# Performance work log

Measured on AMD Instinct MI355X. Metric: run time of the kernel, lower is better.

The kernel has to match this reference:

```python
import jax, jax.numpy as jnp
import numpy as np

B, N, D, P, H, DH = 1, 1536, 512, 64, 16, 64
INNER = H * DH  # 1024

def _ln(x, g, b, eps=1e-5):
    m = jnp.mean(x, axis=-1, keepdims=True)
    v = jnp.var(x, axis=-1, keepdims=True)
    return (x - m) / jnp.sqrt(v + eps) * g + b

def setup_inputs() -> dict:
    key = jax.random.key(0)
    ks = jax.random.split(key, 10)
    s = 0.02
    return {
        "node_feats": jax.random.normal(ks[0], (B, N, D), jnp.float32),
        "pair_feats": jax.random.normal(ks[1], (B, N, N, P), jnp.float32),
        "mask": jnp.ones((B, N, N), dtype=bool),
        "ln_node_g": jnp.ones((D,), jnp.float32), "ln_node_b": jnp.zeros((D,), jnp.float32),
        "ln_pair_g": jnp.ones((P,), jnp.float32), "ln_pair_b": jnp.zeros((P,), jnp.float32),
        "Wq": s * jax.random.normal(ks[2], (D, INNER), jnp.float32),
        "bq": jnp.zeros((INNER,), jnp.float32),
        "Wkv": s * jax.random.normal(ks[3], (D, 2 * INNER), jnp.float32),
        "bkv": jnp.zeros((2 * INNER,), jnp.float32),
        "qln_g": jnp.ones((INNER,), jnp.float32), "qln_b": jnp.zeros((INNER,), jnp.float32),
        "kln_g": jnp.ones((INNER,), jnp.float32), "kln_b": jnp.zeros((INNER,), jnp.float32),
        "Wg": s * jax.random.normal(ks[4], (D, INNER), jnp.float32),
        "bg": jnp.zeros((INNER,), jnp.float32),
        "Wbias": s * jax.random.normal(ks[5], (P, H), jnp.float32),
        "Wout": s * jax.random.normal(ks[6], (INNER, D), jnp.float32),
        "bout": jnp.zeros((D,), jnp.float32),
        "n_queries": 0,
        "n_keys": 0,
    }

def reference(node_feats, pair_feats, mask, ln_node_g, ln_node_b, ln_pair_g, ln_pair_b,
              Wq, bq, Wkv, bkv, qln_g, qln_b, kln_g, kln_b, Wg, bg, Wbias, Wout, bout,
              n_queries, n_keys):
    b, n, _ = node_feats.shape
    x = _ln(node_feats, ln_node_g, ln_node_b)          # [b,n,D]
    p = _ln(pair_feats, ln_pair_g, ln_pair_b)          # [b,n,n,P]
    q = _ln(x @ Wq + bq, qln_g, qln_b)                 # [b,n,I]
    kv = x @ Wkv + bkv
    k, v = jnp.split(kv, 2, axis=-1)
    k = _ln(k, kln_g, kln_b)
    g = x @ Wg + bg                                    # gating, [b,n,I]
    bias = jnp.einsum('bijp,ph->bhij', p, Wbias)       # pair bias, [b,h,n,n]
    # split heads -> [b,h,n,dh]
    split = lambda t: t.reshape(b, n, H, DH).transpose(0, 2, 1, 3)
    qh, kh, vh, gh = split(q), split(k), split(v), split(g)
    scale = DH ** -0.5
    sim = jnp.einsum('bhid,bhjd->bhij', qh, kh) * scale
    sim = jnp.where(mask[:, None, :, :], sim, jnp.finfo(sim.dtype).min)
    attn = jax.nn.softmax(sim + bias, axis=-1)
    o = jnp.einsum('bhij,bhjd->bhid', attn, vh)        # [b,h,n,dh]
    o = jax.nn.sigmoid(gh) * o
    o = o.transpose(0, 2, 1, 3).reshape(b, n, INNER)
    return o @ Wout + bout
```

## Files before the change

### kernel.cpp

```cpp
#include <hip/hip_runtime.h>

#define NN 1536
#define DD 512
#define PP 64
#define HH 16
#define DHD 64
#define INNER 1024
#define NCHUNK 4
#define JT_PER (NN / 64 / NCHUNK)

typedef __attribute__((ext_vector_type(4))) float f32x4;
typedef __attribute__((ext_vector_type(8))) _Float16 f16x8;
typedef __attribute__((ext_vector_type(4))) _Float16 f16x4;

__device__ inline float wave_sum(float v) {
#pragma unroll
  for (int m = 1; m <= 32; m <<= 1) v += __shfl_xor(v, m);
  return v;
}

__global__ __launch_bounds__(256) void prep_kernel(const float* __restrict__ Wq,
    const float* __restrict__ Wkv, const float* __restrict__ Wg,
    const float* __restrict__ Wout, const float* __restrict__ nf,
    const float* __restrict__ lng, const float* __restrict__ lnb,
    _Float16* __restrict__ BTall, _Float16* __restrict__ WoutT,
    _Float16* __restrict__ x16) {
  int bid = blockIdx.x;
  int tid = threadIdx.x;
  if (bid >= 640) {
    int i = bid - 640;
    int c = tid * 2;
    float2 v = *(const float2*)&nf[(size_t)i * DD + c];
    float s = v.x + v.y, ss = v.x * v.x + v.y * v.y;
    s = wave_sum(s); ss = wave_sum(ss);
    __shared__ float red[2][4];
    int w = tid >> 6;
    if ((tid & 63) == 0) { red[0][w] = s; red[1][w] = ss; }
    __syncthreads();
    s = red[0][0] + red[0][1] + red[0][2] + red[0][3];
    ss = red[1][0] + red[1][1] + red[1][2] + red[1][3];
    float mean = s * (1.f / DD);
    float var = ss * (1.f / DD) - mean * mean;
    float rstd = rsqrtf(var + 1e-5f);
    x16[(size_t)i * DD + c + 0] = (_Float16)((v.x - mean) * rstd * lng[c + 0] + lnb[c + 0]);
    x16[(size_t)i * DD + c + 1] = (_Float16)((v.y - mean) * rstd * lng[c + 1] + lnb[c + 1]);
    return;
  }
  const float* src; int Cs, c0, r0, outStride, outCol; _Float16* dst;
  if (bid < 512) {
    int x = bid & 63, y = bid >> 6;
    int cg0 = x * 64; r0 = y * 64;
    if (cg0 < 1024)      { src = Wq;  Cs = 1024; c0 = cg0; }
    else if (cg0 < 3072) { src = Wkv; Cs = 2048; c0 = cg0 - 1024; }
    else                 { src = Wg;  Cs = 1024; c0 = cg0 - 3072; }
    dst = BTall; outStride = DD; outCol = cg0;
  } else {
    int b = bid - 512;
    int x = b & 7, y = b >> 3;
    c0 = x * 64; r0 = y * 64;
    src = Wout; Cs = DD; dst = WoutT; outStride = INNER; outCol = c0;
  }
  __shared__ float tile[64][65];
  int ri = tid >> 4, ci = (tid & 15) * 4;
#pragma unroll
  for (int p = 0; p < 4; ++p) {
    float4 v = *(const float4*)&src[(size_t)(r0 + ri + p * 16) * Cs + c0 + ci];
    tile[ri + p * 16][ci + 0] = v.x;
    tile[ri + p * 16][ci + 1] = v.y;
    tile[ri + p * 16][ci + 2] = v.z;
    tile[ri + p * 16][ci + 3] = v.w;
  }
  __syncthreads();
  int wr = tid >> 3, wc = (tid & 7) * 8;
#pragma unroll
  for (int p = 0; p < 2; ++p) {
    f16x8 o;
#pragma unroll
    for (int jj = 0; jj < 8; ++jj) o[jj] = (_Float16)tile[wc + jj][wr + p * 32];
    *(f16x8*)&dst[(size_t)(outCol + wr + p * 32) * outStride + r0 + wc] = o;
  }
}

__device__ __forceinline__ void pb_body(int i, int jy, int tid,
    const float* __restrict__ pair, const float* __restrict__ pg,
    const float* __restrict__ pb, const float* __restrict__ Wbias,
    _Float16* __restrict__ bias16) {
  int lane = tid & 63, w = tid >> 6;
  int lj = lane & 15, pbase = (lane >> 4) * 8;
  f16x8 wb0, wb1;
#pragma unroll
  for (int jj = 0; jj < 8; ++jj) {
    wb0[jj] = (_Float16)Wbias[(pbase + jj) * HH + lj];
    wb1[jj] = (_Float16)Wbias[(pbase + 32 + jj) * HH + lj];
  }
  float4 g0 = *(const float4*)&pg[pbase],      g1 = *(const float4*)&pg[pbase + 4];
  float4 g2 = *(const float4*)&pg[pbase + 32], g3 = *(const float4*)&pg[pbase + 36];
  float4 b0 = *(const float4*)&pb[pbase],      b1 = *(const float4*)&pb[pbase + 4];
  float4 b2 = *(const float4*)&pb[pbase + 32], b3 = *(const float4*)&pb[pbase + 36];
  __shared__ _Float16 trans[2][16][72];
  int jbase = jy * 256 + w * 16 + lj;
  const float* src = &pair[((size_t)i * NN + jbase) * PP];
  float4 v0 = *(const float4*)&src[pbase];
  float4 v1 = *(const float4*)&src[pbase + 4];
  float4 v2 = *(const float4*)&src[pbase + 32];
  float4 v3 = *(const float4*)&src[pbase + 36];
  for (int t4 = 0; t4 < 4; ++t4) {
    int jt0 = jy * 256 + t4 * 64;
    float4 n0, n1, n2, n3;
    if (t4 < 3) {
      const float* nsrc = &pair[((size_t)i * NN + jbase + (t4 + 1) * 64) * PP];
      n0 = *(const float4*)&nsrc[pbase];
      n1 = *(const float4*)&nsrc[pbase + 4];
      n2 = *(const float4*)&nsrc[pbase + 32];
      n3 = *(const float4*)&nsrc[pbase + 36];
    }
    float s = v0.x + v0.y + v0.z + v0.w + v1.x + v1.y + v1.z + v1.w
            + v2.x + v2.y + v2.z + v2.w + v3.x + v3.y + v3.z + v3.w;
    float ss = v0.x * v0.x + v0.y * v0.y + v0.z * v0.z + v0.w * v0.w
             + v1.x * v1.x + v1.y * v1.y + v1.z * v1.z + v1.w * v1.w
             + v2.x * v2.x + v2.y * v2.y + v2.z * v2.z + v2.w * v2.w
             + v3.x * v3.x + v3.y * v3.y + v3.z * v3.z + v3.w * v3.w;
    s += __shfl_xor(s, 16); s += __shfl_xor(s, 32);
    ss += __shfl_xor(ss, 16); ss += __shfl_xor(ss, 32);
    float mean = s * (1.f / PP);
    float var = ss * (1.f / PP) - mean * mean;
    float rstd = rsqrtf(var + 1e-5f);
    f16x8 a0, a1;
    a0[0] = (_Float16)((v0.x - mean) * rstd * g0.x + b0.x);
    a0[1] = (_Float16)((v0.y - mean) * rstd * g0.y + b0.y);
    a0[2] = (_Float16)((v0.z - mean) * rstd * g0.z + b0.z);
    a0[3] = (_Float16)((v0.w - mean) * rstd * g0.w + b0.w);
    a0[4] = (_Float16)((v1.x - mean) * rstd * g1.x + b1.x);
    a0[5] = (_Float16)((v1.y - mean) * rstd * g1.y + b1.y);
    a0[6] = (_Float16)((v1.z - mean) * rstd * g1.z + b1.z);
    a0[7] = (_Float16)((v1.w - mean) * rstd * g1.w + b1.w);
    a1[0] = (_Float16)((v2.x - mean) * rstd * g2.x + b2.x);
    a1[1] = (_Float16)((v2.y - mean) * rstd * g2.y + b2.y);
    a1[2] = (_Float16)((v2.z - mean) * rstd * g2.z + b2.z);
    a1[3] = (_Float16)((v2.w - mean) * rstd * g2.w + b2.w);
    a1[4] = (_Float16)((v3.x - mean) * rstd * g3.x + b3.x);
    a1[5] = (_Float16)((v3.y - mean) * rstd * g3.y + b3.y);
    a1[6] = (_Float16)((v3.z - mean) * rstd * g3.z + b3.z);
    a1[7] = (_Float16)((v3.w - mean) * rstd * g3.w + b3.w);
    f32x4 cacc = {};
    cacc = __builtin_amdgcn_mfma_f32_16x16x32_f16(a0, wb0, cacc, 0, 0, 0);
    cacc = __builtin_amdgcn_mfma_f32_16x16x32_f16(a1, wb1, cacc, 0, 0, 0);
#pragma unroll
    for (int rg = 0; rg < 4; ++rg)
      trans[t4 & 1][lj][w * 16 + (lane >> 4) * 4 + rg] = (_Float16)cacc[rg];
    __syncthreads();
    int hh = tid >> 4, jc = (tid & 15) * 4;
    f16x4 ov = *(const f16x4*)&trans[t4 & 1][hh][jc];
    *(f16x4*)&bias16[((size_t)hh * NN + i) * NN + jt0 + jc] = ov;
    v0 = n0; v1 = n1; v2 = n2; v3 = n3;
  }
}

__device__ __forceinline__ void gemm_proj_body(int m0, int n0, int tid,
    const _Float16* __restrict__ A, const _Float16* __restrict__ BT,
    const float* __restrict__ bq, const float* __restrict__ bkv,
    const float* __restrict__ bg, _Float16* __restrict__ C) {
  __shared__ _Float16 As[64][72];
  __shared__ _Float16 Bs[64][72];
  int lane = tid & 63, w = tid >> 6;
  int wm = (w & 1) * 32, wn = (w >> 1) * 32;
  f32x4 acc[2][2] = {};
  int r = tid >> 3, c8 = (tid & 7) * 8;
  int lr = lane & 15, lg = lane >> 4;
  for (int k0 = 0; k0 < DD; k0 += 64) {
    *(f16x8*)&As[r][c8]      = *(const f16x8*)&A[(size_t)(m0 + r) * DD + k0 + c8];
    *(f16x8*)&As[r + 32][c8] = *(const f16x8*)&A[(size_t)(m0 + r + 32) * DD + k0 + c8];
    *(f16x8*)&Bs[r][c8]      = *(const f16x8*)&BT[(size_t)(n0 + r) * DD + k0 + c8];
    *(f16x8*)&Bs[r + 32][c8] = *(const f16x8*)&BT[(size_t)(n0 + r + 32) * DD + k0 + c8];
    __syncthreads();
#pragma unroll
    for (int kf = 0; kf < 2; ++kf) {
      f16x8 a0 = *(const f16x8*)&As[wm + lr][kf * 32 + lg * 8];
      f16x8 a1 = *(const f16x8*)&As[wm + 16 + lr][kf * 32 + lg * 8];
      f16x8 b0 = *(const f16x8*)&Bs[wn + lr][kf * 32 + lg * 8];
      f16x8 b1 = *(const f16x8*)&Bs[wn + 16 + lr][kf * 32 + lg * 8];
      acc[0][0] = __builtin_amdgcn_mfma_f32_16x16x32_f16(a0, b0, acc[0][0], 0, 0, 0);
      acc[0][1] = __builtin_amdgcn_mfma_f32_16x16x32_f16(a0, b1, acc[0][1], 0, 0, 0);
      acc[1][0] = __builtin_amdgcn_mfma_f32_16x16x32_f16(a1, b0, acc[1][0], 0, 0, 0);
      acc[1][1] = __builtin_amdgcn_mfma_f32_16x16x32_f16(a1, b1, acc[1][1], 0, 0, 0);
    }
    __syncthreads();
  }
#pragma unroll
  for (int mi = 0; mi < 2; ++mi)
#pragma unroll
    for (int ni = 0; ni < 2; ++ni)
#pragma unroll
      for (int rg = 0; rg < 4; ++rg) {
        int row = m0 + wm + mi * 16 + lg * 4 + rg;
        int col = n0 + wn + ni * 16 + lr;
        float bv = (col < 1024) ? bq[col] : (col < 3072) ? bkv[col - 1024] : bg[col - 3072];
        C[(size_t)row * 4096 + col] = (_Float16)(acc[mi][ni][rg] + bv);
      }
}

__global__ __launch_bounds__(256) void fat_pb_gemm(const float* __restrict__ pair,
    const float* __restrict__ pg, const float* __restrict__ pb,
    const float* __restrict__ Wbias, _Float16* __restrict__ bias16,
    const _Float16* __restrict__ x16, const _Float16* __restrict__ BTall,
    const float* __restrict__ bq, const float* __restrict__ bkv,
    const float* __restrict__ bg, _Float16* __restrict__ prebuf16) {
  int bid = blockIdx.x;
  int g = bid / 7, r = bid - g * 7;
  int tid = threadIdx.x;
  if (r == 6) {
    gemm_proj_body((g >> 6) * 64, (g & 63) * 64, tid, x16, BTall, bq, bkv, bg, prebuf16);
  } else {
    int p = g * 6 + r;
    int jy = p / NN;
    int i = p - jy * NN;
    pb_body(i, jy, tid, pair, pg, pb, Wbias, bias16);
  }
}

__global__ __launch_bounds__(256) void transpose_f16_b(const _Float16* __restrict__ in0,
    _Float16* __restrict__ out0, int R, int C) {
  const _Float16* in = in0 + (size_t)blockIdx.z * R * C;
  _Float16* out = out0 + (size_t)blockIdx.z * R * C;
  __shared__ _Float16 tile[64][72];
  int c0 = blockIdx.x * 64, r0 = blockIdx.y * 64;
  int tid = threadIdx.x;
  int ri = tid >> 3, ci = (tid & 7) * 8;
#pragma unroll
  for (int p = 0; p < 2; ++p)
    *(f16x8*)&tile[ri + p * 32][ci] = *(const f16x8*)&in[(size_t)(r0 + ri + p * 32) * C + c0 + ci];
  __syncthreads();
#pragma unroll
  for (int p = 0; p < 2; ++p) {
    f16x8 o;
#pragma unroll
    for (int jj = 0; jj < 8; ++jj) o[jj] = tile[ci + jj][ri + p * 32];
    *(f16x8*)&out[(size_t)(c0 + ri + p * 32) * R + r0 + ci] = o;
  }
}

__global__ __launch_bounds__(256) void gemm_f16(const _Float16* __restrict__ A,
    const _Float16* __restrict__ BT, const float* __restrict__ bias,
    float* __restrict__ C, int M, int N, int K) {
  __shared__ _Float16 As[64][72];
  __shared__ _Float16 Bs[64][72];
  int tid = threadIdx.x, lane = tid & 63, w = tid >> 6;
  int m0 = blockIdx.y * 64, n0 = blockIdx.x * 64;
  int wm = (w & 1) * 32, wn = (w >> 1) * 32;
  f32x4 acc[2][2] = {};
  int r = tid >> 3, c8 = (tid & 7) * 8;
  int lr = lane & 15, lg = lane >> 4;
  for (int k0 = 0; k0 < K; k0 += 64) {
    *(f16x8*)&As[r][c8]      = *(const f16x8*)&A[(size_t)(m0 + r) * K + k0 + c8];
    *(f16x8*)&As[r + 32][c8] = *(const f16x8*)&A[(size_t)(m0 + r + 32) * K + k0 + c8];
    *(f16x8*)&Bs[r][c8]      = *(const f16x8*)&BT[(size_t)(n0 + r) * K + k0 + c8];
    *(f16x8*)&Bs[r + 32][c8] = *(const f16x8*)&BT[(size_t)(n0 + r + 32) * K + k0 + c8];
    __syncthreads();
#pragma unroll
    for (int kf = 0; kf < 2; ++kf) {
      f16x8 a0 = *(const f16x8*)&As[wm + lr][kf * 32 + lg * 8];
      f16x8 a1 = *(const f16x8*)&As[wm + 16 + lr][kf * 32 + lg * 8];
      f16x8 b0 = *(const f16x8*)&Bs[wn + lr][kf * 32 + lg * 8];
      f16x8 b1 = *(const f16x8*)&Bs[wn + 16 + lr][kf * 32 + lg * 8];
      acc[0][0] = __builtin_amdgcn_mfma_f32_16x16x32_f16(a0, b0, acc[0][0], 0, 0, 0);
      acc[0][1] = __builtin_amdgcn_mfma_f32_16x16x32_f16(a0, b1, acc[0][1], 0, 0, 0);
      acc[1][0] = __builtin_amdgcn_mfma_f32_16x16x32_f16(a1, b0, acc[1][0], 0, 0, 0);
      acc[1][1] = __builtin_amdgcn_mfma_f32_16x16x32_f16(a1, b1, acc[1][1], 0, 0, 0);
    }
    __syncthreads();
  }
#pragma unroll
  for (int mi = 0; mi < 2; ++mi)
#pragma unroll
    for (int ni = 0; ni < 2; ++ni)
#pragma unroll
      for (int rg = 0; rg < 4; ++rg) {
        int row = m0 + wm + mi * 16 + lg * 4 + rg;
        int col = n0 + wn + ni * 16 + lr;
        C[(size_t)row * N + col] = acc[mi][ni][rg] + bias[col];
      }
}

__global__ __launch_bounds__(256) void qkv_ln_kernel(const _Float16* __restrict__ prebuf,
    const float* __restrict__ qg, const float* __restrict__ qb,
    const float* __restrict__ kg, const float* __restrict__ kb,
    _Float16* __restrict__ q16, _Float16* __restrict__ k16, _Float16* __restrict__ v16) {
  int i = blockIdx.x, tid = threadIdx.x;
  int c = tid * 4;
  const _Float16* rowp = &prebuf[(size_t)i * 4096];
  f16x4 qh = *(const f16x4*)&rowp[c];
  f16x4 kh = *(const f16x4*)&rowp[1024 + c];
  f16x4 vh = *(const f16x4*)&rowp[2048 + c];
  float qv[4], kv[4];
#pragma unroll
  for (int e = 0; e < 4; ++e) { qv[e] = (float)qh[e]; kv[e] = (float)kh[e]; }
  float qs = qv[0] + qv[1] + qv[2] + qv[3];
  float qss = qv[0] * qv[0] + qv[1] * qv[1] + qv[2] * qv[2] + qv[3] * qv[3];
  float ks = kv[0] + kv[1] + kv[2] + kv[3];
  float kss = kv[0] * kv[0] + kv[1] * kv[1] + kv[2] * kv[2] + kv[3] * kv[3];
  qs = wave_sum(qs); qss = wave_sum(qss); ks = wave_sum(ks); kss = wave_sum(kss);
  __shared__ float red[4][4];
  int w = tid >> 6;
  if ((tid & 63) == 0) { red[0][w] = qs; red[1][w] = qss; red[2][w] = ks; red[3][w] = kss; }
  __syncthreads();
  qs = red[0][0] + red[0][1] + red[0][2] + red[0][3];
  qss = red[1][0] + red[1][1] + red[1][2] + red[1][3];
  ks = red[2][0] + red[2][1] + red[2][2] + red[2][3];
  kss = red[3][0] + red[3][1] + red[3][2] + red[3][3];
  float qm = qs * (1.f / INNER), qvr = qss * (1.f / INNER) - qm * qm, qr = rsqrtf(qvr + 1e-5f);
  float km = ks * (1.f / INNER), kvr = kss * (1.f / INNER) - km * km, kr = rsqrtf(kvr + 1e-5f);
  int hh = c >> 6, d = c & 63;
  size_t off = ((size_t)hh * NN + i) * DHD + d;
  f16x4 qo, ko;
#pragma unroll
  for (int e = 0; e < 4; ++e) {
    qo[e] = (_Float16)((qv[e] - qm) * qr * qg[c + e] + qb[c + e]);
    ko[e] = (_Float16)((kv[e] - km) * kr * kg[c + e] + kb[c + e]);
  }
  *(f16x4*)&q16[off] = qo;
  *(f16x4*)&k16[off] = ko;
  *(f16x4*)&v16[off] = vh;
}

__global__ __launch_bounds__(256) void attn_kernel(const _Float16* __restrict__ q16,
    const _Float16* __restrict__ k16, const _Float16* __restrict__ vT16,
    const _Float16* __restrict__ bias16, _Float16* __restrict__ opart,
    float* __restrict__ mlbuf) {
  int it = blockIdx.x, h = blockIdx.y, ck = blockIdx.z;
  int tid = threadIdx.x, lane = tid & 63, w = tid >> 6;
  int lr = lane & 15, lg = lane >> 4;
  __shared__ _Float16 Kt[64][72];
  __shared__ _Float16 Vt[64][72];
  int ib0 = it * 64;
  int ib = ib0 + w * 16;
  f16x8 qb0 = *(const f16x8*)&q16[((size_t)h * NN + ib + lr) * DHD + lg * 8];
  f16x8 qb1 = *(const f16x8*)&q16[((size_t)h * NN + ib + lr) * DHD + 32 + lg * 8];
  float m = -INFINITY, lsum = 0.f;
  f32x4 oacc[4] = {};
  int sr = tid >> 3, sc = (tid & 7) * 8;
  int jt0g = ck * JT_PER;
  const _Float16* brow = &bias16[((size_t)h * NN + ib + lr) * NN];
  f16x8 kA, kB, vA, vB;
  {
    int j0 = jt0g * 64;
    kA = *(const f16x8*)&k16[((size_t)h * NN + j0 + sr) * DHD + sc];
    kB = *(const f16x8*)&k16[((size_t)h * NN + j0 + sr + 32) * DHD + sc];
    vA = *(const f16x8*)&vT16[((size_t)h * DHD + sr) * NN + j0 + sc];
    vB = *(const f16x8*)&vT16[((size_t)h * DHD + sr + 32) * NN + j0 + sc];
  }
  for (int jj = 0; jj < JT_PER; ++jj) {
    int j0 = (jt0g + jj) * 64;
    *(f16x8*)&Kt[sr][sc] = kA;
    *(f16x8*)&Kt[sr + 32][sc] = kB;
    *(f16x8*)&Vt[sr][sc] = vA;
    *(f16x8*)&Vt[sr + 32][sc] = vB;
    f16x4 bl[4];
#pragma unroll
    for (int jq = 0; jq < 4; ++jq)
      bl[jq] = *(const f16x4*)&brow[j0 + jq * 16 + lg * 4];
    __syncthreads();
    if (jj + 1 < JT_PER) {
      int j1 = j0 + 64;
      kA = *(const f16x8*)&k16[((size_t)h * NN + j1 + sr) * DHD + sc];
      kB = *(const f16x8*)&k16[((size_t)h * NN + j1 + sr + 32) * DHD + sc];
      vA = *(const f16x8*)&vT16[((size_t)h * DHD + sr) * NN + j1 + sc];
      vB = *(const f16x8*)&vT16[((size_t)h * DHD + sr + 32) * NN + j1 + sc];
    }
    float s[4][4];
#pragma unroll
    for (int jq = 0; jq < 4; ++jq) {
      f16x8 ka0 = *(const f16x8*)&Kt[jq * 16 + lr][lg * 8];
      f16x8 ka1 = *(const f16x8*)&Kt[jq * 16 + lr][32 + lg * 8];
      f32x4 c = {};
      c = __builtin_amdgcn_mfma_f32_16x16x32_f16(ka0, qb0, c, 0, 0, 0);
      c = __builtin_amdgcn_mfma_f32_16x16x32_f16(ka1, qb1, c, 0, 0, 0);
#pragma unroll
      for (int r = 0; r < 4; ++r)
        s[jq][r] = c[r] * 0.125f + (float)bl[jq][r];
    }
    float tmax = s[0][0];
#pragma unroll
    for (int jq = 0; jq < 4; ++jq)
#pragma unroll
      for (int r = 0; r < 4; ++r) tmax = fmaxf(tmax, s[jq][r]);
    tmax = fmaxf(tmax, __shfl_xor(tmax, 16));
    tmax = fmaxf(tmax, __shfl_xor(tmax, 32));
    float mn = fmaxf(m, tmax);
    float alpha = __expf(m - mn);
    float ps = 0.f;
    f16x4 pf[4];
#pragma unroll
    for (int jq = 0; jq < 4; ++jq)
#pragma unroll
      for (int r = 0; r < 4; ++r) {
        float p = __expf(s[jq][r] - mn);
        ps += p;
        pf[jq][r] = (_Float16)p;
      }
    ps += __shfl_xor(ps, 16);
    ps += __shfl_xor(ps, 32);
    lsum = lsum * alpha + ps;
    m = mn;
    float ar[4];
#pragma unroll
    for (int r = 0; r < 4; ++r) ar[r] = __shfl(alpha, lg * 4 + r);
#pragma unroll
    for (int dt = 0; dt < 4; ++dt)
#pragma unroll
      for (int r = 0; r < 4; ++r) oacc[dt][r] *= ar[r];
#pragma unroll
    for (int dt = 0; dt < 4; ++dt)
#pragma unroll
      for (int jq = 0; jq < 4; ++jq) {
        f16x4 vb = *(const f16x4*)&Vt[dt * 16 + lr][jq * 16 + lg * 4];
        oacc[dt] = __builtin_amdgcn_mfma_f32_16x16x16f16(pf[jq], vb, oacc[dt], 0, 0, 0);
      }
    __syncthreads();
  }
  size_t pbase = (((size_t)it * HH + h) * NCHUNK + ck) * 4096 + (size_t)w * 1024;
#pragma unroll
  for (int dt = 0; dt < 4; ++dt) {
    f16x4 ov;
#pragma unroll
    for (int r = 0; r < 4; ++r) ov[r] = (_Float16)oacc[dt][r];
    *(f16x4*)&opart[pbase + dt * 256 + lane * 4] = ov;
  }
  if (lg == 0) {
    size_t mb = (((size_t)it * HH + h) * NCHUNK + ck) * 128;
    mlbuf[mb + w * 16 + lr] = m;
    mlbuf[mb + 64 + w * 16 + lr] = lsum;
  }
}

__global__ __launch_bounds__(256) void attn_merge(const _Float16* __restrict__ opart,
    const float* __restrict__ mlbuf, const _Float16* __restrict__ prebuf,
    _Float16* __restrict__ o16) {
  int it = blockIdx.x, h = blockIdx.y;
  int tid = threadIdx.x, lane = tid & 63, w = tid >> 6;
  int lr = lane & 15, lg = lane >> 4;
  __shared__ float sm[NCHUNK][64], sl[NCHUNK][64];
  {
    int c = tid >> 6, i = tid & 63;
    size_t mb = (((size_t)it * HH + h) * NCHUNK + c) * 128;
    sm[c][i] = mlbuf[mb + i];
    sl[c][i] = mlbuf[mb + 64 + i];
  }
  __syncthreads();
  float wc[NCHUNK][4], linv[4];
#pragma unroll
  for (int r = 0; r < 4; ++r) {
    int i_loc = w * 16 + lg * 4 + r;
    float mg = sm[0][i_loc];
#pragma unroll
    for (int c = 1; c < NCHUNK; ++c) mg = fmaxf(mg, sm[c][i_loc]);
    float lt = 0.f;
#pragma unroll
    for (int c = 0; c < NCHUNK; ++c) {
      float e = __expf(sm[c][i_loc] - mg);
      wc[c][r] = e;
      lt += e * sl[c][i_loc];
    }
    linv[r] = 1.f / lt;
  }
  size_t base = ((size_t)it * HH + h) * NCHUNK * 4096 + (size_t)w * 1024;
#pragma unroll
  for (int dt = 0; dt < 4; ++dt) {
    float o[4] = {};
#pragma unroll
    for (int c = 0; c < NCHUNK; ++c) {
      f16x4 v = *(const f16x4*)&opart[base + (size_t)c * 4096 + dt * 256 + lane * 4];
#pragma unroll
      for (int r = 0; r < 4; ++r) o[r] += wc[c][r] * (float)v[r];
    }
    int d = dt * 16 + lr;
#pragma unroll
    for (int r = 0; r < 4; ++r) {
      int i = it * 64 + w * 16 + lg * 4 + r;
      float gt = (float)prebuf[(size_t)i * 4096 + 3072 + h * DHD + d];
      float val = o[r] * linv[r] * (1.f / (1.f + __expf(-gt)));
      o16[(size_t)i * INNER + h * DHD + d] = (_Float16)val;
    }
  }
}

extern "C" void kernel_launch(void* const* d_in, const int* in_sizes, int n_in,
                              void* d_out, int out_size, void* d_ws, size_t ws_size,
                              hipStream_t stream) {
  const float* node  = (const float*)d_in[0];
  const float* pair  = (const float*)d_in[1];
  const float* ln_ng = (const float*)d_in[3];
  const float* ln_nb = (const float*)d_in[4];
  const float* ln_pg = (const float*)d_in[5];
  const float* ln_pb = (const float*)d_in[6];
  const float* Wq    = (const float*)d_in[7];
  const float* bq    = (const float*)d_in[8];
  const float* Wkv   = (const float*)d_in[9];
  const float* bkv   = (const float*)d_in[10];
  const float* qlg   = (const float*)d_in[11];
  const float* qlb   = (const float*)d_in[12];
  const float* klg   = (const float*)d_in[13];
  const float* klb   = (const float*)d_in[14];
  const float* Wg    = (const float*)d_in[15];
  const float* bg    = (const float*)d_in[16];
  const float* Wbias = (const float*)d_in[17];
  const float* Wout  = (const float*)d_in[18];
  const float* bout  = (const float*)d_in[19];
  float* out = (float*)d_out;

  char* ws = (char*)d_ws;
  const size_t MB = 1u << 20;
  _Float16* BTall    = (_Float16*)(ws + 0 * MB);
  _Float16* WoutT    = (_Float16*)(ws + 4 * MB);
  _Float16* x16      = (_Float16*)(ws + 5 * MB);
  _Float16* prebuf16 = (_Float16*)(ws + 8 * MB);
  _Float16* q16      = (_Float16*)(ws + 20 * MB);
  _Float16* k16      = (_Float16*)(ws + 23 * MB);
  _Float16* v16      = (_Float16*)(ws + 26 * MB);
  _Float16* vT16     = (_Float16*)(ws + 29 * MB);
  _Float16* o16      = (_Float16*)(ws + 32 * MB);
  _Float16* bias16   = (_Float16*)(ws + 36 * MB);
  _Float16* opart    = (_Float16*)(ws + 112 * MB);
  float*    mlbuf    = (float*)(ws + 126 * MB);

  prep_kernel<<<640 + NN, 256, 0, stream>>>(Wq, Wkv, Wg, Wout, node, ln_ng, ln_nb,
                                            BTall, WoutT, x16);
  fat_pb_gemm<<<10752, 256, 0, stream>>>(pair, ln_pg, ln_pb, Wbias, bias16,
                                         x16, BTall, bq, bkv, bg, prebuf16);
  qkv_ln_kernel<<<NN, 256, 0, stream>>>(prebuf16, qlg, qlb, klg, klb, q16, k16, v16);
  transpose_f16_b<<<dim3(1, NN / 64, HH), 256, 0, stream>>>(v16, vT16, NN, DHD);
  attn_kernel<<<dim3(NN / 64, HH, NCHUNK), 256, 0, stream>>>(q16, k16, vT16, bias16, opart, mlbuf);
  attn_merge<<<dim3(NN / 64, HH), 256, 0, stream>>>(opart, mlbuf, prebuf16, o16);
  gemm_f16<<<dim3(DD / 64, NN / 64), 256, 0, stream>>>(o16, WoutT, bout, out, NN, DD, INNER);
}
```

Baseline: 239.6 us.

## Stagger pair-bias computation across fused kernels to overlap with qkv and attention

Splits the pair-bias LN+projection into four j-quarters of 384 columns each and interleaves them with other work in fused launches. The first two quarters run beside the QKV GEMM, the third beside q/k layernorm and the V transpose (now read straight from prebuf), and the fourth beside the first three attention chunks, whose key ranges only need the already-written bias. The aim is to hide the memory-bound pair read behind compute-bound stages and to drop separate launches and the v16 intermediate. This relies on JT_PER=6 matching the 384-column chunking and on block-index ordering for the data dependencies, with added complexity in the block-to-work mapping.

```diff
diff --git a/kernel.cpp b/kernel.cpp
--- a/kernel.cpp
+++ b/kernel.cpp
@@ -7,7 +7,7 @@
 #define DHD 64
 #define INNER 1024
 #define NCHUNK 4
-#define JT_PER (NN / 64 / NCHUNK)
+#define JT_PER 6
 
 typedef __attribute__((ext_vector_type(4))) float f32x4;
 typedef __attribute__((ext_vector_type(8))) _Float16 f16x8;
@@ -81,7 +81,7 @@
   }
 }
 
-__device__ __forceinline__ void pb_body(int i, int jy, int tid,
+__device__ __forceinline__ void pb_body(int i, int q, int tid,
     const float* __restrict__ pair, const float* __restrict__ pg,
     const float* __restrict__ pb, const float* __restrict__ Wbias,
     _Float16* __restrict__ bias16) {
@@ -98,17 +98,17 @@
   float4 b0 = *(const float4*)&pb[pbase],      b1 = *(const float4*)&pb[pbase + 4];
   float4 b2 = *(const float4*)&pb[pbase + 32], b3 = *(const float4*)&pb[pbase + 36];
   __shared__ _Float16 trans[2][16][72];
-  int jbase = jy * 256 + w * 16 + lj;
+  int jbase = q * 384 + w * 16 + lj;
   const float* src = &pair[((size_t)i * NN + jbase) * PP];
   float4 v0 = *(const float4*)&src[pbase];
   float4 v1 = *(const float4*)&src[pbase + 4];
   float4 v2 = *(const float4*)&src[pbase + 32];
   float4 v3 = *(const float4*)&src[pbase + 36];
-  for (int t4 = 0; t4 < 4; ++t4) {
-    int jt0 = jy * 256 + t4 * 64;
+  for (int t = 0; t < 6; ++t) {
+    int jt0 = q * 384 + t * 64;
     float4 n0, n1, n2, n3;
-    if (t4 < 3) {
-      const float* nsrc = &pair[((size_t)i * NN + jbase + (t4 + 1) * 64) * PP];
+    if (t < 5) {
+      const float* nsrc = &pair[((size_t)i * NN + jbase + (t + 1) * 64) * PP];
       n0 = *(const float4*)&nsrc[pbase];
       n1 = *(const float4*)&nsrc[pbase + 4];
       n2 = *(const float4*)&nsrc[pbase + 32];
@@ -147,10 +147,10 @@
     cacc = __builtin_amdgcn_mfma_f32_16x16x32_f16(a1, wb1, cacc, 0, 0, 0);
 #pragma unroll
     for (int rg = 0; rg < 4; ++rg)
-      trans[t4 & 1][lj][w * 16 + (lane >> 4) * 4 + rg] = (_Float16)cacc[rg];
+      trans[t & 1][lj][w * 16 + (lane >> 4) * 4 + rg] = (_Float16)cacc[rg];
     __syncthreads();
     int hh = tid >> 4, jc = (tid & 15) * 4;
-    f16x4 ov = *(const f16x4*)&trans[t4 & 1][hh][jc];
+    f16x4 ov = *(const f16x4*)&trans[t & 1][hh][jc];
     *(f16x4*)&bias16[((size_t)hh * NN + i) * NN + jt0 + jc] = ov;
     v0 = n0; v1 = n1; v2 = n2; v3 = n3;
   }
@@ -199,98 +199,15 @@
       }
 }
 
-__global__ __launch_bounds__(256) void fat_pb_gemm(const float* __restrict__ pair,
-    const float* __restrict__ pg, const float* __restrict__ pb,
-    const float* __restrict__ Wbias, _Float16* __restrict__ bias16,
-    const _Float16* __restrict__ x16, const _Float16* __restrict__ BTall,
-    const float* __restrict__ bq, const float* __restrict__ bkv,
-    const float* __restrict__ bg, _Float16* __restrict__ prebuf16) {
-  int bid = blockIdx.x;
-  int g = bid / 7, r = bid - g * 7;
-  int tid = threadIdx.x;
-  if (r == 6) {
-    gemm_proj_body((g >> 6) * 64, (g & 63) * 64, tid, x16, BTall, bq, bkv, bg, prebuf16);
-  } else {
-    int p = g * 6 + r;
-    int jy = p / NN;
-    int i = p - jy * NN;
-    pb_body(i, jy, tid, pair, pg, pb, Wbias, bias16);
-  }
-}
-
-__global__ __launch_bounds__(256) void transpose_f16_b(const _Float16* __restrict__ in0,
-    _Float16* __restrict__ out0, int R, int C) {
-  const _Float16* in = in0 + (size_t)blockIdx.z * R * C;
-  _Float16* out = out0 + (size_t)blockIdx.z * R * C;
-  __shared__ _Float16 tile[64][72];
-  int c0 = blockIdx.x * 64, r0 = blockIdx.y * 64;
-  int tid = threadIdx.x;
-  int ri = tid >> 3, ci = (tid & 7) * 8;
-#pragma unroll
-  for (int p = 0; p < 2; ++p)
-    *(f16x8*)&tile[ri + p * 32][ci] = *(const f16x8*)&in[(size_t)(r0 + ri + p * 32) * C + c0 + ci];
-  __syncthreads();
-#pragma unroll
-  for (int p = 0; p < 2; ++p) {
-    f16x8 o;
-#pragma unroll
-    for (int jj = 0; jj < 8; ++jj) o[jj] = tile[ci + jj][ri + p * 32];
-    *(f16x8*)&out[(size_t)(c0 + ri + p * 32) * R + r0 + ci] = o;
-  }
-}
-
-__global__ __launch_bounds__(256) void gemm_f16(const _Float16* __restrict__ A,
-    const _Float16* __restrict__ BT, const float* __restrict__ bias,
-    float* __restrict__ C, int M, int N, int K) {
-  __shared__ _Float16 As[64][72];
-  __shared__ _Float16 Bs[64][72];
-  int tid = threadIdx.x, lane = tid & 63, w = tid >> 6;
-  int m0 = blockIdx.y * 64, n0 = blockIdx.x * 64;
-  int wm = (w & 1) * 32, wn = (w >> 1) * 32;
-  f32x4 acc[2][2] = {};
-  int r = tid >> 3, c8 = (tid & 7) * 8;
-  int lr = lane & 15, lg = lane >> 4;
-  for (int k0 = 0; k0 < K; k0 += 64) {
-    *(f16x8*)&As[r][c8]      = *(const f16x8*)&A[(size_t)(m0 + r) * K + k0 + c8];
-    *(f16x8*)&As[r + 32][c8] = *(const f16x8*)&A[(size_t)(m0 + r + 32) * K + k0 + c8];
-    *(f16x8*)&Bs[r][c8]      = *(const f16x8*)&BT[(size_t)(n0 + r) * K + k0 + c8];
-    *(f16x8*)&Bs[r + 32][c8] = *(const f16x8*)&BT[(size_t)(n0 + r + 32) * K + k0 + c8];
-    __syncthreads();
-#pragma unroll
-    for (int kf = 0; kf < 2; ++kf) {
-      f16x8 a0 = *(const f16x8*)&As[wm + lr][kf * 32 + lg * 8];
-      f16x8 a1 = *(const f16x8*)&As[wm + 16 + lr][kf * 32 + lg * 8];
-      f16x8 b0 = *(const f16x8*)&Bs[wn + lr][kf * 32 + lg * 8];
-      f16x8 b1 = *(const f16x8*)&Bs[wn + 16 + lr][kf * 32 + lg * 8];
-      acc[0][0] = __builtin_amdgcn_mfma_f32_16x16x32_f16(a0, b0, acc[0][0], 0, 0, 0);
-      acc[0][1] = __builtin_amdgcn_mfma_f32_16x16x32_f16(a0, b1, acc[0][1], 0, 0, 0);
-      acc[1][0] = __builtin_amdgcn_mfma_f32_16x16x32_f16(a1, b0, acc[1][0], 0, 0, 0);
-      acc[1][1] = __builtin_amdgcn_mfma_f32_16x16x32_f16(a1, b1, acc[1][1], 0, 0, 0);
-    }
-    __syncthreads();
-  }
-#pragma unroll
-  for (int mi = 0; mi < 2; ++mi)
-#pragma unroll
-    for (int ni = 0; ni < 2; ++ni)
-#pragma unroll
-      for (int rg = 0; rg < 4; ++rg) {
-        int row = m0 + wm + mi * 16 + lg * 4 + rg;
-        int col = n0 + wn + ni * 16 + lr;
-        C[(size_t)row * N + col] = acc[mi][ni][rg] + bias[col];
-      }
-}
-
-__global__ __launch_bounds__(256) void qkv_ln_kernel(const _Float16* __restrict__ prebuf,
+__device__ __forceinline__ void qkv_body(int i, int tid,
+    const _Float16* __restrict__ prebuf,
     const float* __restrict__ qg, const float* __restrict__ qb,
     const float* __restrict__ kg, const float* __restrict__ kb,
-    _Float16* __restrict__ q16, _Float16* __restrict__ k16, _Float16* __restrict__ v16) {
-  int i = blockIdx.x, tid = threadIdx.x;
+    _Float16* __restrict__ q16, _Float16* __restrict__ k16) {
   int c = tid * 4;
   const _Float16* rowp = &prebuf[(size_t)i * 4096];
   f16x4 qh = *(const f16x4*)&rowp[c];
   f16x4 kh = *(const f16x4*)&rowp[1024 + c];
-  f16x4 vh = *(const f16x4*)&rowp[2048 + c];
   float qv[4], kv[4];
 #pragma unroll
   for (int e = 0; e < 4; ++e) { qv[e] = (float)qh[e]; kv[e] = (float)kh[e]; }
@@ -319,15 +236,33 @@
   }
   *(f16x4*)&q16[off] = qo;
   *(f16x4*)&k16[off] = ko;
-  *(f16x4*)&v16[off] = vh;
-}
-
-__global__ __launch_bounds__(256) void attn_kernel(const _Float16* __restrict__ q16,
-    const _Float16* __restrict__ k16, const _Float16* __restrict__ vT16,
-    const _Float16* __restrict__ bias16, _Float16* __restrict__ opart,
-    float* __restrict__ mlbuf) {
-  int it = blockIdx.x, h = blockIdx.y, ck = blockIdx.z;
-  int tid = threadIdx.x, lane = tid & 63, w = tid >> 6;
+}
+
+__device__ __forceinline__ void vt_body(int t, int tid,
+    const _Float16* __restrict__ prebuf, _Float16* __restrict__ vT16) {
+  int z = t / 24, y = t - z * 24;
+  __shared__ _Float16 tile[64][72];
+  int r0 = y * 64;
+  int ri = tid >> 3, ci = (tid & 7) * 8;
+#pragma unroll
+  for (int p = 0; p < 2; ++p)
+    *(f16x8*)&tile[ri + p * 32][ci] =
+        *(const f16x8*)&prebuf[(size_t)(r0 + ri + p * 32) * 4096 + 2048 + z * 64 + ci];
+  __syncthreads();
+#pragma unroll
+  for (int p = 0; p < 2; ++p) {
+    f16x8 o;
+#pragma unroll
+    for (int jj = 0; jj < 8; ++jj) o[jj] = tile[ci + jj][ri + p * 32];
+    *(f16x8*)&vT16[((size_t)z * DHD + ri + p * 32) * NN + r0 + ci] = o;
+  }
+}
+
+__device__ __forceinline__ void attn_body(int it, int h, int ck, int tid,
+    const _Float16* __restrict__ q16, const _Float16* __restrict__ k16,
+    const _Float16* __restrict__ vT16, const _Float16* __restrict__ bias16,
+    _Float16* __restrict__ opart, float* __restrict__ mlbuf) {
+  int lane = tid & 63, w = tid >> 6;
   int lr = lane & 15, lg = lane >> 4;
   __shared__ _Float16 Kt[64][72];
   __shared__ _Float16 Vt[64][72];
@@ -432,6 +367,68 @@
   }
 }
 
+__global__ __launch_bounds__(256) void fat2(const float* __restrict__ pair,
+    const float* __restrict__ pg, const float* __restrict__ pb,
+    const float* __restrict__ Wbias, _Float16* __restrict__ bias16,
+    const _Float16* __restrict__ x16, const _Float16* __restrict__ BTall,
+    const float* __restrict__ bq, const float* __restrict__ bkv,
+    const float* __restrict__ bg, _Float16* __restrict__ prebuf16) {
+  int bid = blockIdx.x;
+  int g = bid / 3, r = bid - g * 3;
+  int tid = threadIdx.x;
+  if (r == 2) {
+    gemm_proj_body((g >> 6) * 64, (g & 63) * 64, tid, x16, BTall, bq, bkv, bg, prebuf16);
+  } else {
+    int p = g * 2 + r;
+    pb_body(p % NN, p / NN, tid, pair, pg, pb, Wbias, bias16);
+  }
+}
+
+__global__ __launch_bounds__(256) void fat3(const float* __restrict__ pair,
+    const float* __restrict__ pg, const float* __restrict__ pb,
+    const float* __restrict__ Wbias, _Float16* __restrict__ bias16,
+    const _Float16* __restrict__ prebuf16,
+    const float* __restrict__ qg, const float* __restrict__ qb,
+    const float* __restrict__ kg, const float* __restrict__ kb,
+    _Float16* __restrict__ q16, _Float16* __restrict__ k16,
+    _Float16* __restrict__ vT16) {
+  int bid = blockIdx.x;
+  int g = bid / 9, r = bid - g * 9;
+  int tid = threadIdx.x;
+  if (r < 4) {
+    pb_body(g * 4 + r, 2, tid, pair, pg, pb, Wbias, bias16);
+  } else if (r < 8) {
+    qkv_body(g * 4 + (r - 4), tid, prebuf16, qg, qb, kg, kb, q16, k16);
+  } else {
+    vt_body(g, tid, prebuf16, vT16);
+  }
+}
+
+__global__ __launch_bounds__(256) void fat4(const float* __restrict__ pair,
+    const float* __restrict__ pg, const float* __restrict__ pb,
+    const float* __restrict__ Wbias, _Float16* __restrict__ bias16,
+    const _Float16* __restrict__ q16, const _Float16* __restrict__ k16,
+    const _Float16* __restrict__ vT16, _Float16* __restrict__ opart,
+    float* __restrict__ mlbuf) {
+  int bid = blockIdx.x;
+  int g = bid / 7, r = bid - g * 7;
+  int tid = threadIdx.x;
+  if (r < 4) {
+    pb_body(g * 4 + r, 3, tid, pair, pg, pb, Wbias, bias16);
+  } else {
+    int a = g * 3 + (r - 4);
+    int ck = a % 3, h = (a / 3) % 16, it = a / 48;
+    attn_body(it, h, ck, tid, q16, k16, vT16, bias16, opart, mlbuf);
+  }
+}
+
+__global__ __launch_bounds__(256) void attn_last(const _Float16* __restrict__ q16,
+    const _Float16* __restrict__ k16, const _Float16* __restrict__ vT16,
+    const _Float16* __restrict__ bias16, _Float16* __restrict__ opart,
+    float* __restrict__ mlbuf) {
+  attn_body(blockIdx.x, blockIdx.y, 3, threadIdx.x, q16, k16, vT16, bias16, opart, mlbuf);
+}
+
 __global__ __launch_bounds__(256) void attn_merge(const _Float16* __restrict__ opart,
     const float* __restrict__ mlbuf, const _Float16* __restrict__ prebuf,
     _Float16* __restrict__ o16) {
@@ -481,6 +478,48 @@
       o16[(size_t)i * INNER + h * DHD + d] = (_Float16)val;
     }
   }
+}
+
+__global__ __launch_bounds__(256) void gemm_f16(const _Float16* __restrict__ A,
+    const _Float16* __restrict__ BT, const float* __restrict__ bias,
+    float* __restrict__ C, int M, int N, int K) {
+  __shared__ _Float16 As[64][72];
+  __shared__ _Float16 Bs[64][72];
+  int tid = threadIdx.x, lane = tid & 63, w = tid >> 6;
+  int m0 = blockIdx.y * 64, n0 = blockIdx.x * 64;
+  int wm = (w & 1) * 32, wn = (w >> 1) * 32;
+  f32x4 acc[2][2] = {};
+  int r = tid >> 3, c8 = (tid & 7) * 8;
+  int lr = lane & 15, lg = lane >> 4;
+  for (int k0 = 0; k0 < K; k0 += 64) {
+    *(f16x8*)&As[r][c8]      = *(const f16x8*)&A[(size_t)(m0 + r) * K + k0 + c8];
+    *(f16x8*)&As[r + 32][c8] = *(const f16x8*)&A[(size_t)(m0 + r + 32) * K + k0 + c8];
+    *(f16x8*)&Bs[r][c8]      = *(const f16x8*)&BT[(size_t)(n0 + r) * K + k0 + c8];
+    *(f16x8*)&Bs[r + 32][c8] = *(const f16x8*)&BT[(size_t)(n0 + r + 32) * K + k0 + c8];
+    __syncthreads();
+#pragma unroll
+    for (int kf = 0; kf < 2; ++kf) {
+      f16x8 a0 = *(const f16x8*)&As[wm + lr][kf * 32 + lg * 8];
+      f16x8 a1 = *(const f16x8*)&As[wm + 16 + lr][kf * 32 + lg * 8];
+      f16x8 b0 = *(const f16x8*)&Bs[wn + lr][kf * 32 + lg * 8];
+      f16x8 b1 = *(const f16x8*)&Bs[wn + 16 + lr][kf * 32 + lg * 8];
+      acc[0][0] = __builtin_amdgcn_mfma_f32_16x16x32_f16(a0, b0, acc[0][0], 0, 0, 0);
+      acc[0][1] = __builtin_amdgcn_mfma_f32_16x16x32_f16(a0, b1, acc[0][1], 0, 0, 0);
+      acc[1][0] = __builtin_amdgcn_mfma_f32_16x16x32_f16(a1, b0, acc[1][0], 0, 0, 0);
+      acc[1][1] = __builtin_amdgcn_mfma_f32_16x16x32_f16(a1, b1, acc[1][1], 0, 0, 0);
+    }
+    __syncthreads();
+  }
+#pragma unroll
+  for (int mi = 0; mi < 2; ++mi)
+#pragma unroll
+    for (int ni = 0; ni < 2; ++ni)
+#pragma unroll
+      for (int rg = 0; rg < 4; ++rg) {
+        int row = m0 + wm + mi * 16 + lg * 4 + rg;
+        int col = n0 + wn + ni * 16 + lr;
+        C[(size_t)row * N + col] = acc[mi][ni][rg] + bias[col];
+      }
 }
 
 extern "C" void kernel_launch(void* const* d_in, const int* in_sizes, int n_in,
@@ -515,7 +554,6 @@
   _Float16* prebuf16 = (_Float16*)(ws + 8 * MB);
   _Float16* q16      = (_Float16*)(ws + 20 * MB);
   _Float16* k16      = (_Float16*)(ws + 23 * MB);
-  _Float16* v16      = (_Float16*)(ws + 26 * MB);
   _Float16* vT16     = (_Float16*)(ws + 29 * MB);
   _Float16* o16      = (_Float16*)(ws + 32 * MB);
   _Float16* bias16   = (_Float16*)(ws + 36 * MB);
@@ -524,11 +562,13 @@
 
   prep_kernel<<<640 + NN, 256, 0, stream>>>(Wq, Wkv, Wg, Wout, node, ln_ng, ln_nb,
                                             BTall, WoutT, x16);
-  fat_pb_gemm<<<10752, 256, 0, stream>>>(pair, ln_pg, ln_pb, Wbias, bias16,
-                                         x16, BTall, bq, bkv, bg, prebuf16);
-  qkv_ln_kernel<<<NN, 256, 0, stream>>>(prebuf16, qlg, qlb, klg, klb, q16, k16, v16);
-  transpose_f16_b<<<dim3(1, NN / 64, HH), 256, 0, stream>>>(v16, vT16, NN, DHD);
-  attn_kernel<<<dim3(NN / 64, HH, NCHUNK), 256, 0, stream>>>(q16, k16, vT16, bias16, opart, mlbuf);
+  fat2<<<4608, 256, 0, stream>>>(pair, ln_pg, ln_pb, Wbias, bias16,
+                                 x16, BTall, bq, bkv, bg, prebuf16);
+  fat3<<<3456, 256, 0, stream>>>(pair, ln_pg, ln_pb, Wbias, bias16,
+                                 prebuf16, qlg, qlb, klg, klb, q16, k16, vT16);
+  fat4<<<2688, 256, 0, stream>>>(pair, ln_pg, ln_pb, Wbias, bias16,
+                                 q16, k16, vT16, opart, mlbuf);
+  attn_last<<<dim3(NN / 64, HH), 256, 0, stream>>>(q16, k16, vT16, bias16, opart, mlbuf);
   attn_merge<<<dim3(NN / 64, HH), 256, 0, stream>>>(opart, mlbuf, prebuf16, o16);
   gemm_f16<<<dim3(DD / 64, NN / 64), 256, 0, stream>>>(o16, WoutT, bout, out, NN, DD, INNER);
 }
```

Result: no change. 240.9 us (+0.5%).
